# Kernel tuning notes

Hardware: AMD Instinct MI355X
Metric: run time of the kernel (lower is better)

Reference implementation:

```python
import jax, jax.numpy as jnp
import numpy as np

HIDDEN = 2048
HEADS = 16
HEAD_DIM = HIDDEN // HEADS
LATENT = 512
B, T = 2, 2048


def setup_inputs() -> dict:
    key = jax.random.key(0)
    ks = jax.random.split(key, 12)
    s = lambda fan_in: 1.0 / np.sqrt(fan_in)
    x = jax.random.normal(ks[0], (B, T, HIDDEN), dtype=jnp.float32)
    Wq = jax.random.uniform(ks[1], (HIDDEN, HIDDEN), jnp.float32, -s(HIDDEN), s(HIDDEN))
    bq = jax.random.uniform(ks[2], (HIDDEN,), jnp.float32, -s(HIDDEN), s(HIDDEN))
    Wl = jax.random.uniform(ks[3], (HIDDEN, LATENT), jnp.float32, -s(HIDDEN), s(HIDDEN))
    bl = jax.random.uniform(ks[4], (LATENT,), jnp.float32, -s(HIDDEN), s(HIDDEN))
    # per-head back-projections stacked along head axis: [H, latent, head_dim]
    Wk = jax.random.uniform(ks[5], (HEADS, LATENT, HEAD_DIM), jnp.float32, -s(LATENT), s(LATENT))
    bk = jax.random.uniform(ks[6], (HEADS, HEAD_DIM), jnp.float32, -s(LATENT), s(LATENT))
    Wv = jax.random.uniform(ks[7], (HEADS, LATENT, HEAD_DIM), jnp.float32, -s(LATENT), s(LATENT))
    bv = jax.random.uniform(ks[8], (HEADS, HEAD_DIM), jnp.float32, -s(LATENT), s(LATENT))
    Wo = jax.random.uniform(ks[9], (HIDDEN, HIDDEN), jnp.float32, -s(HIDDEN), s(HIDDEN))
    bo = jax.random.uniform(ks[10], (HIDDEN,), jnp.float32, -s(HIDDEN), s(HIDDEN))
    return {"x": x, "Wq": Wq, "bq": bq, "Wl": Wl, "bl": bl,
            "Wk": Wk, "bk": bk, "Wv": Wv, "bv": bv, "Wo": Wo, "bo": bo}


def reference(x, Wq, bq, Wl, bl, Wk, bk, Wv, bv, Wo, bo):
    Bc, Tc, _ = x.shape
    # Q projection, split into heads: [B, H, T, Dh]
    q = (x @ Wq + bq).reshape(Bc, Tc, HEADS, HEAD_DIM).transpose(0, 2, 1, 3)
    # shared low-rank latent KV (cache=None -> just new tokens): [B, T, L]
    latent = x @ Wl + bl
    # per-head back-projections fused as one grouped matmul: [B, H, T, Dh]
    k = jnp.einsum('btl,hld->bhtd', latent, Wk) + bk[None, :, None, :]
    v = jnp.einsum('btl,hld->bhtd', latent, Wv) + bv[None, :, None, :]
    # full (non-causal) attention, matching the original module
    scores = jnp.einsum('bhqd,bhkd->bhqk', q, k) / np.sqrt(HEAD_DIM).astype(jnp.float32)
    probs = jax.nn.softmax(scores, axis=-1)
    attn = jnp.einsum('bhqk,bhkd->bhqd', probs, v)
    attn = attn.transpose(0, 2, 1, 3).reshape(Bc, Tc, HIDDEN)
    return attn @ Wo + bo
```

## Files before the change

### kernel.cpp

```cpp
#include <hip/hip_runtime.h>
#include <hip/hip_bf16.h>
#include <cstdint>

#define SEQ     2048
#define NHID    2048
#define NLAT    512
#define NHEAD   16
#define DHEAD   128
#define NBATCH  2
#define NROWS   (NBATCH*SEQ)

typedef unsigned short u16;
typedef __attribute__((ext_vector_type(8))) short short8;
typedef __attribute__((ext_vector_type(4))) float f32x4;

#define MFMA16 __builtin_amdgcn_mfma_f32_16x16x32_bf16

#define QSCALE 0.12751743f

#if __has_builtin(__builtin_amdgcn_exp2f)
#define EXP2(x) __builtin_amdgcn_exp2f(x)
#else
#define EXP2(x) __expf((x) * 0.6931471805599453f)
#endif

__device__ __forceinline__ u16 f2b(float f) {
    uint32_t u = __float_as_uint(f);
    uint32_t r = (u + 0x7fffu + ((u >> 16) & 1u)) >> 16;
    return (u16)r;
}

__device__ __forceinline__ uint32_t cvt_pk_bf16(float a, float b) {
    uint32_t r;
    asm("v_cvt_pk_bf16_f32 %0, %1, %2" : "=v"(r) : "v"(a), "v"(b));
    return r;
}

__device__ __forceinline__ void async16(const u16* g, u16* l) {
    __builtin_amdgcn_global_load_lds(
        (const __attribute__((address_space(1))) unsigned int*)g,
        (__attribute__((address_space(3))) unsigned int*)l, 16, 0, 0);
}

__device__ __forceinline__ void stage_lds(const u16* __restrict__ src, size_t strideE,
                                          u16* lds, int wave, int lane,
                                          int log2cpr, int xmask, int xshift,
                                          int reps, int nlanes) {
    const int cmask = (1 << log2cpr) - 1;
    for (int rep = 0; rep < reps; ++rep) {
        int cbase = rep * nlanes + wave * 64;
        int ci = cbase + lane;
        int row = ci >> log2cpr;
        int sc = ci & cmask;
        int dchunk = sc ^ ((row >> xshift) & xmask);
        const u16* g = src + (size_t)row * strideE + dchunk * 8;
        async16(g, lds + (size_t)cbase * 8);
    }
}

__global__ __launch_bounds__(256) void prep(const float* __restrict__ x,
                                            const float* __restrict__ Wq,
                                            const float* __restrict__ Wl,
                                            const float* __restrict__ Wk,
                                            const float* __restrict__ Wv,
                                            const float* __restrict__ Wo,
                                            u16* __restrict__ xb,
                                            u16* __restrict__ WqlT,
                                            u16* __restrict__ WkvT,
                                            u16* __restrict__ WoT) {
    const int t = blockIdx.x, tid = threadIdx.x;
    if (t < 8192) {
        int i = t * 256 + tid;
        float4 v = ((const float4*)x)[i];
        unsigned int lo = (unsigned int)f2b(v.x) | ((unsigned int)f2b(v.y) << 16);
        unsigned int hi = (unsigned int)f2b(v.z) | ((unsigned int)f2b(v.w) << 16);
        ((uint2*)xb)[i] = make_uint2(lo, hi);
        return;
    }
    __shared__ float tile[32][33];
    const float* src; u16* dst; int R, C, tY, tX;
    if (t < 12288)      { int tt = t - 8192;  src = Wq; dst = WqlT;           R = 2048; C = 2048; tY = tt >> 6; tX = tt & 63; }
    else if (t < 13312) { int tt = t - 12288; src = Wl; dst = WqlT + 4194304; R = 2048; C = 512;  tY = tt >> 4; tX = tt & 15; }
    else if (t < 14336) { int tt = t - 13312; int hh = tt >> 6; tt &= 63;
                          src = Wk + hh * 65536; dst = WkvT + hh * 65536;     R = 512;  C = 128;  tY = tt >> 2; tX = tt & 3; }
    else if (t < 15360) { int tt = t - 14336; int hh = tt >> 6; tt &= 63;
                          src = Wv + hh * 65536; dst = WkvT + 1048576 + hh * 65536;
                                                                              R = 512;  C = 128;  tY = tt >> 2; tX = tt & 3; }
    else                { int tt = t - 15360; src = Wo; dst = WoT;            R = 2048; C = 2048; tY = tt >> 6; tX = tt & 63; }
    const int r0 = tY * 32, c0 = tX * 32;
    {
        const int rr = tid >> 3, c4 = tid & 7;
        float4 v4 = *(const float4*)&src[(size_t)(r0 + rr) * C + c0 + c4 * 4];
        tile[rr][c4 * 4 + 0] = v4.x;
        tile[rr][c4 * 4 + 1] = v4.y;
        tile[rr][c4 * 4 + 2] = v4.z;
        tile[rr][c4 * 4 + 3] = v4.w;
    }
    __syncthreads();
    {
        const int rg = tid & 7, cc = tid >> 3;
        ushort4 o4;
        o4.x = f2b(tile[rg * 4 + 0][cc]);
        o4.y = f2b(tile[rg * 4 + 1][cc]);
        o4.z = f2b(tile[rg * 4 + 2][cc]);
        o4.w = f2b(tile[rg * 4 + 3][cc]);
        *(ushort4*)&dst[(size_t)(c0 + cc) * R + r0 + rg * 4] = o4;
    }
}

template<int STORE>
__global__ __launch_bounds__(256) void gemm_bt(const u16* __restrict__ A,
                                               const u16* __restrict__ Bt,
                                               const float* __restrict__ bias1,
                                               const float* __restrict__ bias2,
                                               void* __restrict__ C1,
                                               void* __restrict__ C2,
                                               int M, int N, int K) {
    __shared__ __align__(16) u16 As[2][128 * 32];
    __shared__ __align__(16) u16 Bs[2][128 * 32];
    const int tid = threadIdx.x, wave = tid >> 6, lane = tid & 63;
    const int quad = lane >> 4, m16 = lane & 15;
    const int gx = gridDim.x;
    const int nwg = gx * gridDim.y;
    int lin = blockIdx.x + gx * blockIdx.y;
    int xcd = lin & 7, pos = lin >> 3;
    int qq = nwg >> 3, rr2 = nwg & 7;
    int wg = (xcd < rr2) ? xcd * (qq + 1) + pos
                         : rr2 * (qq + 1) + (xcd - rr2) * qq + pos;
    const int m0 = (wg / gx) * 128, n0 = (wg % gx) * 128;
    const int wr = wave >> 1, wc = wave & 1;
    const int swz = (quad ^ ((m16 >> 1) & 3)) * 8;
    const u16* Ab = A + (size_t)m0 * K;
    const u16* Bb = Bt + (size_t)n0 * K;
    const int KI = K >> 5;

    stage_lds(Ab, K, As[0], wave, lane, 2, 3, 1, 2, 256);
    stage_lds(Bb, K, Bs[0], wave, lane, 2, 3, 1, 2, 256);

    f32x4 acc[4][4] = {};
    for (int it = 0; it < KI; ++it) {
        const int cur = it & 1;
        __syncthreads();
        if (it + 1 < KI) {
            stage_lds(Ab + (it + 1) * 32, K, As[cur ^ 1], wave, lane, 2, 3, 1, 2, 256);
            stage_lds(Bb + (it + 1) * 32, K, Bs[cur ^ 1], wave, lane, 2, 3, 1, 2, 256);
        }
        short8 af[4], bfr[4];
        #pragma unroll
        for (int i = 0; i < 4; i++)
            af[i] = *(const short8*)&As[cur][(wr * 64 + i * 16 + m16) * 32 + swz];
        #pragma unroll
        for (int j = 0; j < 4; j++)
            bfr[j] = *(const short8*)&Bs[cur][(wc * 64 + j * 16 + m16) * 32 + swz];
        #pragma unroll
        for (int i = 0; i < 4; i++)
            #pragma unroll
            for (int j = 0; j < 4; j++)
                acc[i][j] = MFMA16(af[i], bfr[j], acc[i][j], 0, 0, 0);
    }
    const bool second = (n0 >= 2048);
    #pragma unroll
    for (int j = 0; j < 4; j++) {
        int n = n0 + wc * 64 + j * 16 + m16;
        float bv;
        if constexpr (STORE == 2) bv = bias1[n];
        else bv = second ? bias2[n - 2048] : bias1[n];
        #pragma unroll
        for (int i = 0; i < 4; i++) {
            int mrow = m0 + wr * 64 + i * 16 + quad * 4;
            if constexpr (STORE == 4) {
                if (second) {
                    int n2 = n - 2048;
                    ushort4 pkv;
                    pkv.x = f2b(acc[i][j][0] + bv);
                    pkv.y = f2b(acc[i][j][1] + bv);
                    pkv.z = f2b(acc[i][j][2] + bv);
                    pkv.w = f2b(acc[i][j][3] + bv);
                    int c = mrow & 2047;
                    c = (c & ~12) | ((c & 4) << 1) | ((c & 8) >> 1);
                    *(ushort4*)&((u16*)C2)[((size_t)((m0 >> 11) * 2048 + n2)) * 2048 + c] = pkv;
                    continue;
                }
            }
            #pragma unroll
            for (int r = 0; r < 4; r++) {
                float v = acc[i][j][r] + bv;
                int m = mrow + r;
                if constexpr (STORE == 2)
                    ((float*)C1)[(size_t)m * N + n] = v;
                else if constexpr (STORE == 3) {
                    if (!second) ((u16*)C1)[(size_t)m * 2048 + n] = f2b(v * QSCALE);
                    else         ((u16*)C2)[(size_t)m * 512 + (n - 2048)] = f2b(v);
                } else {
                    ((u16*)C1)[(size_t)m * 2048 + n] = f2b(v);
                }
            }
        }
    }
}

__global__ __launch_bounds__(256, 2) void attn_fused(const u16* __restrict__ Q,
                                                     const u16* __restrict__ Kf,
                                                     const u16* __restrict__ Vt,
                                                     u16* __restrict__ Ob) {
    __shared__ __align__(16) u16 Kt[2][64 * 128];
    __shared__ __align__(16) u16 Vtile[2][128 * 64];
    const int tid = threadIdx.x, wave = tid >> 6, lane = tid & 63;
    const int quad = lane >> 4, m16 = lane & 15;
    const int bh = blockIdx.x, b = bh >> 4, h = bh & 15;
    const int q0 = blockIdx.y * 128;
    const size_t grow = (size_t)b * SEQ;
    const u16* Kbase = Kf + grow * NHID + h * DHEAD;
    const u16* Vbase = Vt + (grow + h * DHEAD) * SEQ;

    const u16* qsrc = Q + (grow + q0) * NHID + h * DHEAD;
    stage_lds(qsrc, NHID, Kt[0], wave, lane, 4, 15, 0, 4, 256);
    stage_lds(qsrc + (size_t)64 * NHID, NHID, Kt[1], wave, lane, 4, 15, 0, 4, 256);
    __syncthreads();
    short8 qf[2][4];
    {
        const u16* qbuf = Kt[wave >> 1];
        int rbase = (wave & 1) * 32;
        #pragma unroll
        for (int i = 0; i < 2; i++)
            #pragma unroll
            for (int c = 0; c < 4; c++)
                qf[i][c] = *(const short8*)&qbuf[(rbase + i * 16 + m16) * 128 +
                                                (((c * 4 + quad) ^ m16)) * 8];
    }
    __syncthreads();

    stage_lds(Kbase, NHID, Kt[0], wave, lane, 4, 15, 0, 4, 256);
    stage_lds(Vbase, SEQ, Vtile[0], wave, lane, 3, 7, 0, 4, 256);

    f32x4 o[2][8] = {};
    float lsum[2] = {};

    for (int it = 0; it < SEQ / 64; ++it) {
        const int cur = it & 1;
        __syncthreads();
        if (it + 1 < SEQ / 64) {
            stage_lds(Kbase + (size_t)(it + 1) * 64 * NHID, NHID, Kt[cur ^ 1],
                      wave, lane, 4, 15, 0, 4, 256);
            stage_lds(Vbase + (it + 1) * 64, SEQ, Vtile[cur ^ 1],
                      wave, lane, 3, 7, 0, 4, 256);
        }
        const u16* kt = Kt[cur];
        const u16* vt = Vtile[cur];

        f32x4 s[2][4] = {};
        __builtin_amdgcn_s_setprio(1);
        #pragma unroll
        for (int c = 0; c < 4; c++)
            #pragma unroll
            for (int j = 0; j < 4; j++) {
                short8 kb = *(const short8*)&kt[(j * 16 + m16) * 128 +
                                               (((c * 4 + quad) ^ m16)) * 8];
                s[0][j] = MFMA16(kb, qf[0][c], s[0][j], 0, 0, 0);
                s[1][j] = MFMA16(kb, qf[1][c], s[1][j], 0, 0, 0);
            }
        __builtin_amdgcn_s_setprio(0);

        uint32_t pk[2][4][2];
        #pragma unroll
        for (int i = 0; i < 2; i++) {
            float rs = 0.f;
            #pragma unroll
            for (int j = 0; j < 4; j++) {
                float p0 = EXP2(s[i][j][0]);
                float p1 = EXP2(s[i][j][1]);
                float p2 = EXP2(s[i][j][2]);
                float p3 = EXP2(s[i][j][3]);
                rs += (p0 + p1) + (p2 + p3);
                pk[i][j][0] = cvt_pk_bf16(p0, p1);
                pk[i][j][1] = cvt_pk_bf16(p2, p3);
            }
            lsum[i] += rs;
        }

        __builtin_amdgcn_s_setprio(1);
        #pragma unroll
        for (int c2 = 0; c2 < 2; c2++) {
            short8 pa[2];
            #pragma unroll
            for (int i = 0; i < 2; i++) {
                union { uint32_t u[4]; short8 s8; } pu;
#if __has_builtin(__builtin_amdgcn_permlane32_swap)
                auto r0 = __builtin_amdgcn_permlane32_swap(pk[i][2 * c2][0],
                                                           pk[i][2 * c2 + 1][0],
                                                           false, false);
                auto r1 = __builtin_amdgcn_permlane32_swap(pk[i][2 * c2][1],
                                                           pk[i][2 * c2 + 1][1],
                                                           false, false);
                pu.u[0] = r0[0]; pu.u[1] = r1[0]; pu.u[2] = r0[1]; pu.u[3] = r1[1];
#else
                uint32_t jl0 = pk[i][2 * c2][0],     jl1 = pk[i][2 * c2][1];
                uint32_t jh0 = pk[i][2 * c2 + 1][0], jh1 = pk[i][2 * c2 + 1][1];
                uint32_t sl0 = __shfl_xor(jl0, 32), sl1 = __shfl_xor(jl1, 32);
                uint32_t sh0 = __shfl_xor(jh0, 32), sh1 = __shfl_xor(jh1, 32);
                const bool low = lane < 32;
                pu.u[0] = low ? jl0 : sh0;
                pu.u[1] = low ? jl1 : sh1;
                pu.u[2] = low ? sl0 : jh0;
                pu.u[3] = low ? sl1 : jh1;
#endif
                pa[i] = pu.s8;
            }
            #pragma unroll
            for (int jd = 0; jd < 8; jd++) {
                short8 vb = *(const short8*)&vt[(jd * 16 + m16) * 64 +
                                               (((c2 * 4 + quad) ^ (m16 & 7))) * 8];
                o[0][jd] = MFMA16(pa[0], vb, o[0][jd], 0, 0, 0);
                o[1][jd] = MFMA16(pa[1], vb, o[1][jd], 0, 0, 0);
            }
        }
        __builtin_amdgcn_s_setprio(0);
    }

    #pragma unroll
    for (int i = 0; i < 2; i++) {
        float v = lsum[i];
        v += __shfl_xor(v, 16);
        v += __shfl_xor(v, 32);
        lsum[i] = v;
    }
    #pragma unroll
    for (int i = 0; i < 2; i++) {
        float inv[4];
        #pragma unroll
        for (int r = 0; r < 4; r++)
            inv[r] = 1.f / __shfl(lsum[i], quad * 4 + r);
        #pragma unroll
        for (int jd = 0; jd < 8; jd++)
            #pragma unroll
            for (int r = 0; r < 4; r++) {
                int t = q0 + wave * 32 + i * 16 + quad * 4 + r;
                int d = jd * 16 + m16;
                Ob[(grow + t) * NHID + h * DHEAD + d] = f2b(o[i][jd][r] * inv[r]);
            }
    }
}

extern "C" void kernel_launch(void* const* d_in, const int* in_sizes, int n_in,
                              void* d_out, int out_size, void* d_ws, size_t ws_size,
                              hipStream_t stream) {
    const float* x  = (const float*)d_in[0];
    const float* Wq = (const float*)d_in[1];
    const float* bq = (const float*)d_in[2];
    const float* Wl = (const float*)d_in[3];
    const float* bl = (const float*)d_in[4];
    const float* Wk = (const float*)d_in[5];
    const float* bk = (const float*)d_in[6];
    const float* Wv = (const float*)d_in[7];
    const float* bv = (const float*)d_in[8];
    const float* Wo = (const float*)d_in[9];
    const float* bo = (const float*)d_in[10];
    float* out = (float*)d_out;

    u16* w = (u16*)d_ws;
    u16* xb    = w;
    u16* WqlT  = xb    + 8388608;
    u16* WkvT  = WqlT  + 5242880;
    u16* WoT   = WkvT  + 2097152;
    u16* qb    = WoT   + 4194304;
    u16* kb    = qb    + 8388608;
    u16* vt    = kb    + 8388608;
    u16* lat   = vt    + 8388608;
    u16* attnb = xb;

    prep<<<19456, 256, 0, stream>>>(x, Wq, Wl, Wk, Wv, Wo, xb, WqlT, WkvT, WoT);

    gemm_bt<3><<<dim3(20, 32), 256, 0, stream>>>(xb, WqlT, bq, bl, qb, lat,
                                                 NROWS, 2560, 2048);
    gemm_bt<4><<<dim3(32, 32), 256, 0, stream>>>(lat, WkvT, bk, bv, kb, vt,
                                                 NROWS, 4096, 512);

    attn_fused<<<dim3(32, 16), 256, 0, stream>>>(qb, kb, vt, attnb);

    gemm_bt<2><<<dim3(16, 32), 256, 0, stream>>>(attnb, WoT, bo, nullptr, out, nullptr,
                                                 NROWS, 2048, 2048);
}
```

Measured before the change: 334.1 us.

## Single-buffer V tile via register prefetch to fit three blocks per CU

The attention kernel's V tile drops from two LDS buffers to one. The next V tile is prefetched into registers with plain global loads and written to LDS at the top of each iteration, behind an extra barrier. Launch bounds rise from 2 to 3 blocks per CU, aiming for more occupancy now that LDS use per block is lower. In exchange, each iteration gets one more __syncthreads, registers are capped more tightly (possible spills), and the V load latency is exposed differently.

```diff
diff --git a/kernel.cpp b/kernel.cpp
--- a/kernel.cpp
+++ b/kernel.cpp
@@ -199,12 +199,12 @@
     }
 }
 
-__global__ __launch_bounds__(256, 2) void attn_fused(const u16* __restrict__ Q,
+__global__ __launch_bounds__(256, 3) void attn_fused(const u16* __restrict__ Q,
                                                      const u16* __restrict__ Kf,
                                                      const u16* __restrict__ Vt,
                                                      u16* __restrict__ Ob) {
     __shared__ __align__(16) u16 Kt[2][64 * 128];
-    __shared__ __align__(16) u16 Vtile[2][128 * 64];
+    __shared__ __align__(16) u16 Vtile[128 * 64];
     const int tid = threadIdx.x, wave = tid >> 6, lane = tid & 63;
     const int quad = lane >> 4, m16 = lane & 15;
     const int bh = blockIdx.x, b = bh >> 4, h = bh & 15;
@@ -230,23 +230,45 @@
     }
     __syncthreads();
 
+    const int ci0 = wave * 64 + lane;
+    const int ci1 = ci0 + 256, ci2 = ci0 + 512, ci3 = ci0 + 768;
+    const u16* vsrc0 = Vbase + (size_t)(ci0 >> 3) * SEQ + ((ci0 & 7) ^ ((ci0 >> 3) & 7)) * 8;
+    const u16* vsrc1 = Vbase + (size_t)(ci1 >> 3) * SEQ + ((ci1 & 7) ^ ((ci1 >> 3) & 7)) * 8;
+    const u16* vsrc2 = Vbase + (size_t)(ci2 >> 3) * SEQ + ((ci2 & 7) ^ ((ci2 >> 3) & 7)) * 8;
+    const u16* vsrc3 = Vbase + (size_t)(ci3 >> 3) * SEQ + ((ci3 & 7) ^ ((ci3 >> 3) & 7)) * 8;
+    u16* vdst0 = &Vtile[ci0 * 8];
+    u16* vdst1 = &Vtile[ci1 * 8];
+    u16* vdst2 = &Vtile[ci2 * 8];
+    u16* vdst3 = &Vtile[ci3 * 8];
+
     stage_lds(Kbase, NHID, Kt[0], wave, lane, 4, 15, 0, 4, 256);
-    stage_lds(Vbase, SEQ, Vtile[0], wave, lane, 3, 7, 0, 4, 256);
+    float4 v0 = *(const float4*)vsrc0;
+    float4 v1 = *(const float4*)vsrc1;
+    float4 v2 = *(const float4*)vsrc2;
+    float4 v3 = *(const float4*)vsrc3;
 
     f32x4 o[2][8] = {};
     float lsum[2] = {};
 
     for (int it = 0; it < SEQ / 64; ++it) {
         const int cur = it & 1;
+        __syncthreads();
+        *(float4*)vdst0 = v0;
+        *(float4*)vdst1 = v1;
+        *(float4*)vdst2 = v2;
+        *(float4*)vdst3 = v3;
         __syncthreads();
         if (it + 1 < SEQ / 64) {
             stage_lds(Kbase + (size_t)(it + 1) * 64 * NHID, NHID, Kt[cur ^ 1],
                       wave, lane, 4, 15, 0, 4, 256);
-            stage_lds(Vbase + (it + 1) * 64, SEQ, Vtile[cur ^ 1],
-                      wave, lane, 3, 7, 0, 4, 256);
+            const int off = (it + 1) * 64;
+            v0 = *(const float4*)(vsrc0 + off);
+            v1 = *(const float4*)(vsrc1 + off);
+            v2 = *(const float4*)(vsrc2 + off);
+            v3 = *(const float4*)(vsrc3 + off);
         }
         const u16* kt = Kt[cur];
-        const u16* vt = Vtile[cur];
+        const u16* vt = Vtile;
 
         f32x4 s[2][4] = {};
         __builtin_amdgcn_s_setprio(1);
```

Result: slower. 387.2 us (+15.9%).

## Add triple-buffered LDS pipeline to GEMMs and transpose MFMA for V store

Applied to the files above, without the earlier changes.

Adds a three-buffer LDS pipeline for the large-K GEMMs (Q/latent projection and output projection). It keeps two tiles in flight, uses explicit vmcnt waits instead of a full syncthreads, and raises wave priority around the MFMA block. For the V half of the KV GEMM it swaps the MFMA operands so each lane's accumulator runs along the other dimension, then rewrites the transposed V store as scalar stores. The extra buffer raises LDS use per block, which may lower occupancy, and the vmcnt(4) count assumes stage_lds issues exactly a fixed number of loads.

```diff
diff --git a/kernel.cpp b/kernel.cpp
--- a/kernel.cpp
+++ b/kernel.cpp
@@ -108,7 +108,40 @@
     }
 }
 
-template<int STORE>
+#define GEMM_K_STEP(CUR)                                                        \
+    do {                                                                        \
+        const int swz_ = (quad ^ ((m16 >> 1) & 3)) * 8;                         \
+        short8 af_[4], bf_[4];                                                  \
+        _Pragma("unroll")                                                       \
+        for (int i_ = 0; i_ < 4; i_++)                                          \
+            af_[i_] = *(const short8*)&As[CUR][(wr * 64 + i_ * 16 + m16) * 32 + swz_]; \
+        _Pragma("unroll")                                                       \
+        for (int j_ = 0; j_ < 4; j_++)                                          \
+            bf_[j_] = *(const short8*)&Bs[CUR][(wc * 64 + j_ * 16 + m16) * 32 + swz_]; \
+        if constexpr (STORE == 4) {                                             \
+            if (second) {   \
+                _Pragma("unroll")                                               \
+                for (int i_ = 0; i_ < 4; i_++)                                  \
+                    _Pragma("unroll")                                           \
+                    for (int j_ = 0; j_ < 4; j_++)                              \
+                        acc[i_][j_] = MFMA16(bf_[j_], af_[i_], acc[i_][j_], 0, 0, 0); \
+            } else {                                                            \
+                _Pragma("unroll")                                               \
+                for (int i_ = 0; i_ < 4; i_++)                                  \
+                    _Pragma("unroll")                                           \
+                    for (int j_ = 0; j_ < 4; j_++)                              \
+                        acc[i_][j_] = MFMA16(af_[i_], bf_[j_], acc[i_][j_], 0, 0, 0); \
+            }                                                                   \
+        } else {                                                                \
+            _Pragma("unroll")                                                   \
+            for (int i_ = 0; i_ < 4; i_++)                                      \
+                _Pragma("unroll")                                               \
+                for (int j_ = 0; j_ < 4; j_++)                                  \
+                    acc[i_][j_] = MFMA16(af_[i_], bf_[j_], acc[i_][j_], 0, 0, 0); \
+        }                                                                       \
+    } while (0)
+
+template<int STORE, int NBUF>
 __global__ __launch_bounds__(256) void gemm_bt(const u16* __restrict__ A,
                                                const u16* __restrict__ Bt,
                                                const float* __restrict__ bias1,
@@ -116,8 +149,8 @@
                                                void* __restrict__ C1,
                                                void* __restrict__ C2,
                                                int M, int N, int K) {
-    __shared__ __align__(16) u16 As[2][128 * 32];
-    __shared__ __align__(16) u16 Bs[2][128 * 32];
+    __shared__ __align__(16) u16 As[NBUF][128 * 32];
+    __shared__ __align__(16) u16 Bs[NBUF][128 * 32];
     const int tid = threadIdx.x, wave = tid >> 6, lane = tid & 63;
     const int quad = lane >> 4, m16 = lane & 15;
     const int gx = gridDim.x;
@@ -129,36 +162,74 @@
                          : rr2 * (qq + 1) + (xcd - rr2) * qq + pos;
     const int m0 = (wg / gx) * 128, n0 = (wg % gx) * 128;
     const int wr = wave >> 1, wc = wave & 1;
-    const int swz = (quad ^ ((m16 >> 1) & 3)) * 8;
     const u16* Ab = A + (size_t)m0 * K;
     const u16* Bb = Bt + (size_t)n0 * K;
     const int KI = K >> 5;
-
-    stage_lds(Ab, K, As[0], wave, lane, 2, 3, 1, 2, 256);
-    stage_lds(Bb, K, Bs[0], wave, lane, 2, 3, 1, 2, 256);
+    const bool second = (n0 >= 2048);
+
+    auto stage = [&](const u16* src, u16* buf) {
+        stage_lds(src, K, buf, wave, lane, 2, 3, 1, 2, 256);
+    };
 
     f32x4 acc[4][4] = {};
-    for (int it = 0; it < KI; ++it) {
-        const int cur = it & 1;
-        __syncthreads();
-        if (it + 1 < KI) {
-            stage_lds(Ab + (it + 1) * 32, K, As[cur ^ 1], wave, lane, 2, 3, 1, 2, 256);
-            stage_lds(Bb + (it + 1) * 32, K, Bs[cur ^ 1], wave, lane, 2, 3, 1, 2, 256);
-        }
-        short8 af[4], bfr[4];
-        #pragma unroll
-        for (int i = 0; i < 4; i++)
-            af[i] = *(const short8*)&As[cur][(wr * 64 + i * 16 + m16) * 32 + swz];
-        #pragma unroll
-        for (int j = 0; j < 4; j++)
-            bfr[j] = *(const short8*)&Bs[cur][(wc * 64 + j * 16 + m16) * 32 + swz];
-        #pragma unroll
-        for (int i = 0; i < 4; i++)
-            #pragma unroll
-            for (int j = 0; j < 4; j++)
-                acc[i][j] = MFMA16(af[i], bfr[j], acc[i][j], 0, 0, 0);
-    }
-    const bool second = (n0 >= 2048);
+
+    if constexpr (NBUF == 2) {
+        stage(Ab, As[0]);
+        stage(Bb, Bs[0]);
+        for (int it = 0; it < KI; ++it) {
+            const int cur = it & 1;
+            __syncthreads();
+            if (it + 1 < KI) {
+                stage(Ab + (it + 1) * 32, As[cur ^ 1]);
+                stage(Bb + (it + 1) * 32, Bs[cur ^ 1]);
+            }
+            GEMM_K_STEP(cur);
+        }
+    } else {
+        stage(Ab, As[0]);
+        stage(Bb, Bs[0]);
+        stage(Ab + 32, As[1]);
+        stage(Bb + 32, Bs[1]);
+        int bcur = 0;
+        for (int it = 0; it < KI; ++it) {
+            if (it + 1 < KI) asm volatile("s_waitcnt vmcnt(4)" ::: "memory");
+            else             asm volatile("s_waitcnt vmcnt(0)" ::: "memory");
+            __builtin_amdgcn_s_barrier();
+            asm volatile("" ::: "memory");
+            if (it + 2 < KI) {
+                int bn = bcur + 2; if (bn >= 3) bn -= 3;
+                stage(Ab + (it + 2) * 32, As[bn]);
+                stage(Bb + (it + 2) * 32, Bs[bn]);
+            }
+            __builtin_amdgcn_s_setprio(1);
+            GEMM_K_STEP(bcur);
+            __builtin_amdgcn_s_setprio(0);
+            bcur = (bcur == 2) ? 0 : bcur + 1;
+        }
+    }
+
+    if constexpr (STORE == 4) {
+        if (second) {
+            const int m16s = (m16 & 3) | ((m16 & 4) << 1) | ((m16 & 8) >> 1);
+            const int n2b = (n0 - 2048) + wc * 64 + quad * 4;
+            const size_t rowbase = (size_t)(m0 >> 11) * 2048;
+            const int colbase = (m0 & 2047) + wr * 64 + m16s;
+            #pragma unroll
+            for (int j = 0; j < 4; j++) {
+                #pragma unroll
+                for (int r = 0; r < 4; r++) {
+                    const int n2 = n2b + j * 16 + r;
+                    const float bv = bias2[n2];
+                    #pragma unroll
+                    for (int i = 0; i < 4; i++)
+                        ((u16*)C2)[(rowbase + n2) * 2048 + colbase + i * 16] =
+                            f2b(acc[i][j][r] + bv);
+                }
+            }
+            return;
+        }
+    }
+
     #pragma unroll
     for (int j = 0; j < 4; j++) {
         int n = n0 + wc * 64 + j * 16 + m16;
@@ -168,20 +239,6 @@
         #pragma unroll
         for (int i = 0; i < 4; i++) {
             int mrow = m0 + wr * 64 + i * 16 + quad * 4;
-            if constexpr (STORE == 4) {
-                if (second) {
-                    int n2 = n - 2048;
-                    ushort4 pkv;
-                    pkv.x = f2b(acc[i][j][0] + bv);
-                    pkv.y = f2b(acc[i][j][1] + bv);
-                    pkv.z = f2b(acc[i][j][2] + bv);
-                    pkv.w = f2b(acc[i][j][3] + bv);
-                    int c = mrow & 2047;
-                    c = (c & ~12) | ((c & 4) << 1) | ((c & 8) >> 1);
-                    *(ushort4*)&((u16*)C2)[((size_t)((m0 >> 11) * 2048 + n2)) * 2048 + c] = pkv;
-                    continue;
-                }
-            }
             #pragma unroll
             for (int r = 0; r < 4; r++) {
                 float v = acc[i][j][r] + bv;
@@ -370,13 +427,13 @@
 
     prep<<<19456, 256, 0, stream>>>(x, Wq, Wl, Wk, Wv, Wo, xb, WqlT, WkvT, WoT);
 
-    gemm_bt<3><<<dim3(20, 32), 256, 0, stream>>>(xb, WqlT, bq, bl, qb, lat,
-                                                 NROWS, 2560, 2048);
-    gemm_bt<4><<<dim3(32, 32), 256, 0, stream>>>(lat, WkvT, bk, bv, kb, vt,
-                                                 NROWS, 4096, 512);
+    gemm_bt<3, 3><<<dim3(20, 32), 256, 0, stream>>>(xb, WqlT, bq, bl, qb, lat,
+                                                    NROWS, 2560, 2048);
+    gemm_bt<4, 2><<<dim3(32, 32), 256, 0, stream>>>(lat, WkvT, bk, bv, kb, vt,
+                                                    NROWS, 4096, 512);
 
     attn_fused<<<dim3(32, 16), 256, 0, stream>>>(qb, kb, vt, attnb);
 
-    gemm_bt<2><<<dim3(16, 32), 256, 0, stream>>>(attnb, WoT, bo, nullptr, out, nullptr,
-                                                 NROWS, 2048, 2048);
-}
+    gemm_bt<2, 3><<<dim3(16, 32), 256, 0, stream>>>(attnb, WoT, bo, nullptr, out, nullptr,
+                                                    NROWS, 2048, 2048);
+}
```

Result: slower. 344.5 us (+3.1%).
